# Performance work log

Measured on AMD Instinct MI355X. Metric: run time of the kernel, lower is better.

Reference implementation:

```python
import jax, jax.numpy as jnp
import numpy as np

B, T, C, L = 256, 512, 512, 64  # batch, timesteps, num_classes (blank = C-1), max label len
NEG = -1e30   # log-space 'minus infinity' that is safe under fp arithmetic
EPS = 1e-7    # keras.backend.epsilon() used by ctc_batch_cost


def _ctc_loss(log_probs, labels, in_len, lab_len, blank):
    """CTC negative log-likelihood via the forward (alpha) DP in log space.
    log_probs: [T, B, C] log probabilities; labels: [B, L] int; in_len, lab_len: [B] int.
    Returns [B] loss. Matches tf.nn.ctc_loss with merge_repeated=True, blank=C-1."""
    Tn, Bn, Cn = log_probs.shape
    Ln = labels.shape[1]
    S = 2 * Ln + 1  # extended label: blank, l1, blank, l2, ..., blank
    ext = jnp.full((Bn, S), blank, dtype=labels.dtype).at[:, 1::2].set(labels)  # [B,S]
    # skip transition s-2 -> s allowed iff ext[s] != blank and ext[s] != ext[s-2]
    allow = jnp.concatenate(
        [jnp.zeros((Bn, 2), dtype=bool),
         (ext[:, 2:] != blank) & (ext[:, 2:] != ext[:, :-2])], axis=1)  # [B,S]
    # emission log-probs for each extended-label position at every step: [T,B,S]
    emit = log_probs[:, jnp.arange(Bn)[:, None], ext]

    alpha0 = (jnp.full((Bn, S), NEG, dtype=log_probs.dtype)
              .at[:, 0].set(emit[0, :, 0])
              .at[:, 1].set(emit[0, :, 1]))

    def step(alpha, e):
        a1 = jnp.pad(alpha, ((0, 0), (1, 0)), constant_values=NEG)[:, :-1]
        a2 = jnp.pad(alpha, ((0, 0), (2, 0)), constant_values=NEG)[:, :-2]
        a2 = jnp.where(allow, a2, NEG)
        new = jax.nn.logsumexp(jnp.stack([alpha, a1, a2], axis=0), axis=0) + e
        return new, new

    _, alphas = jax.lax.scan(step, alpha0, emit[1:])
    alphas = jnp.concatenate([alpha0[None], alphas], axis=0)  # [T,B,S]
    # alpha at the last valid timestep of each sample
    final = alphas[in_len - 1, jnp.arange(Bn)]  # [B,S]
    i1 = (2 * lab_len)[:, None]       # last blank position
    i2 = (2 * lab_len - 1)[:, None]   # last label position
    last = jnp.concatenate(
        [jnp.take_along_axis(final, i1, axis=1),
         jnp.take_along_axis(final, i2, axis=1)], axis=1)  # [B,2]
    return -jax.nn.logsumexp(last, axis=1)  # [B]


def setup_inputs() -> dict:
    key = jax.random.key(0)
    k1, k2 = jax.random.split(key)
    # model output is a softmax distribution over classes (keras ctc_batch_cost contract)
    y_pred = jax.nn.softmax(jax.random.normal(k1, (B, T, C), dtype=jnp.float32), axis=-1)
    y_true = jax.random.randint(k2, (B, L), 0, C - 1, dtype=jnp.int32)  # never blank (C-1)
    input_length = jnp.full((B, 1), T, dtype=jnp.int32)
    label_length = jnp.full((B, 1), L, dtype=jnp.int32)
    return {"y_true": y_true, "y_pred": y_pred,
            "input_length": input_length, "label_length": label_length}


def reference(y_true, y_pred, input_length, label_length):
    # keras.backend.ctc_batch_cost: log(transpose(y_pred) + eps), blank = num_classes-1
    log_probs = jnp.log(jnp.transpose(y_pred, (1, 0, 2)) + EPS)  # [T,B,C]
    loss = _ctc_loss(log_probs, y_true, input_length[:, 0], label_length[:, 0], C - 1)
    return loss[:, None]  # [B,1], matching ctc_batch_cost
```

## Files before the change

### kernel.cpp

```cpp
#include <hip/hip_runtime.h>


constexpr int Bc = 256, Tc = 512, Cc = 512, Lc = 64;
constexpr int BLANK = Cc - 1;
constexpr float EPSF = 1e-7f;
constexpr float NEGI = -1e30f;
constexpr float LN2 = 0.6931471805599453f;
constexpr int SR = 64;
constexpr int NSEG = Tc / SR;
constexpr int NW = 8;
constexpr int NPROD = NW - 1;

__device__ __forceinline__ float exp2_hw(float x) { return __builtin_amdgcn_exp2f(x); }
__device__ __forceinline__ float log2_hw(float x) { return __builtin_amdgcn_logf(x); }

__device__ __forceinline__ float lse2(float a, float b) {
    float m = fmaxf(a, b);
    return m + log2_hw(exp2_hw(a - m) + exp2_hw(b - m));
}
__device__ __forceinline__ float lse3(float a, float b, float c) {
    float m = fmaxf(fmaxf(a, b), c);
    return m + log2_hw(exp2_hw(a - m) + exp2_hw(b - m) + exp2_hw(c - m));
}

__global__ __launch_bounds__(NW * 64, 1) void ctc_fwd(
    const int* __restrict__ labels,
    const float* __restrict__ yp,
    const int* __restrict__ in_len,
    const int* __restrict__ lab_len,
    float* __restrict__ out)
{
    __shared__ float sL[2][SR * 64];
    __shared__ float sB[2][SR];

    const int b = blockIdx.x;
    const int tid = threadIdx.x;
    const int lane = tid & 63;
    const int wave = tid >> 6;

    const float* __restrict__ row0 = yp + (size_t)b * (size_t)(Tc * Cc);

    const int lab = labels[b * Lc + lane];
    const int labPrev = __shfl_up(lab, 1);
    const bool allow = (lane >= 1 && lab != BLANK && lab != labPrev);

    int til = in_len[b];  if (til > Tc) til = Tc;
    const int lln = lab_len[b];

    auto fillRow = [&](int buf, int t, int r) {
        float v  = row0[(size_t)t * Cc + lab];
        float vb = row0[(size_t)t * Cc + BLANK];
        sL[buf][r * 64 + lane] = log2_hw(v + EPSF);
        if (lane == 0) sB[buf][r] = log2_hw(vb + EPSF);
    };

    #pragma unroll 2
    for (int r = wave; r < SR; r += NW) fillRow(0, r, r);

    float aB, aL, aH = NEGI;
    {
        float eb0 = log2_hw(row0[BLANK] + EPSF);
        float el0 = log2_hw(row0[lab] + EPSF);
        aB = (lane == 0) ? eb0 : NEGI;
        aL = (lane == 0) ? el0 : NEGI;
    }

    __syncthreads();

    for (int s = 0; s < NSEG; ++s) {
        const int buf = s & 1;
        if (wave == 0) {
            #pragma unroll 8
            for (int k = 0; k < SR; ++k) {
                int t = s * SR + k;
                float el = sL[buf][k * 64 + lane];
                float eb = sB[buf][k];

                float lp = __shfl_up(aL, 1);
                lp = (lane == 0) ? NEGI : lp;
                float lpm = allow ? lp : NEGI;

                float nB = lse2(aB, lp) + eb;
                float nL = lse3(aL, aB, lpm) + el;
                float nH = lse2(aH, aL) + eb;
                if (t >= 1 && t < til) { aB = nB; aL = nL; aH = nH; }
            }
        } else if (s + 1 < NSEG) {
            const int tb = (s + 1) * SR;
            #pragma unroll 2
            for (int r = wave - 1; r < SR; r += NPROD) fillRow(buf ^ 1, tb + r, r);
        }
        __syncthreads();
    }

    if (wave == 0) {
        float v1a = __shfl(aB, lln & 63);
        float v1b = __shfl(aH, 63);
        float v1 = (lln >= 64) ? v1b : v1a;
        float v2 = (lln >= 1) ? __shfl(aL, (lln - 1) & 63) : NEGI;
        if (lane == 0) out[b] = -LN2 * lse2(v1, v2);
    }
}

extern "C" void kernel_launch(void* const* d_in, const int* in_sizes, int n_in,
                              void* d_out, int out_size, void* d_ws, size_t ws_size,
                              hipStream_t stream) {
    const int*   y_true       = (const int*)d_in[0];
    const float* y_pred       = (const float*)d_in[1];
    const int*   input_length = (const int*)d_in[2];
    const int*   label_length = (const int*)d_in[3];
    float*       out          = (float*)d_out;

    ctc_fwd<<<Bc, NW * 64, 0, stream>>>(y_true, y_pred, input_length, label_length, out);
}
```

Before: 387.8 us.

## Stage full probability rows via coalesced float4 loads into shared memory

Replaces the scattered per-label gathers from global memory with all 512 threads streaming whole time-step rows (16 steps × 512 classes) into a double-buffered shared tile using coalesced float4 loads held in registers. The DP wave then gathers label and blank probabilities from shared memory and computes the log itself. Segment length drops from 64 to 16. The change reads the full row (8x more bytes than needed) and adds more syncs, in exchange for coalesced access and no uncoalesced gather latency. It also moves the log computation onto the serial DP path.

```diff
diff --git a/kernel.cpp b/kernel.cpp
--- a/kernel.cpp
+++ b/kernel.cpp
@@ -6,10 +6,11 @@
 constexpr float EPSF = 1e-7f;
 constexpr float NEGI = -1e30f;
 constexpr float LN2 = 0.6931471805599453f;
-constexpr int SR = 64;
+constexpr int SR = 16;
 constexpr int NSEG = Tc / SR;
-constexpr int NW = 8;
-constexpr int NPROD = NW - 1;
+constexpr int NT = 512;
+constexpr int F4_SEG = SR * Cc / 4;
+constexpr int F4_THR = F4_SEG / NT;
 
 __device__ __forceinline__ float exp2_hw(float x) { return __builtin_amdgcn_exp2f(x); }
 __device__ __forceinline__ float log2_hw(float x) { return __builtin_amdgcn_logf(x); }
@@ -23,15 +24,14 @@
     return m + log2_hw(exp2_hw(a - m) + exp2_hw(b - m) + exp2_hw(c - m));
 }
 
-__global__ __launch_bounds__(NW * 64, 1) void ctc_fwd(
+__global__ __launch_bounds__(NT, 1) void ctc_fwd(
     const int* __restrict__ labels,
     const float* __restrict__ yp,
     const int* __restrict__ in_len,
     const int* __restrict__ lab_len,
     float* __restrict__ out)
 {
-    __shared__ float sL[2][SR * 64];
-    __shared__ float sB[2][SR];
+    __shared__ float F[2][SR * Cc];
 
     const int b = blockIdx.x;
     const int tid = threadIdx.x;
@@ -47,18 +47,15 @@
     int til = in_len[b];  if (til > Tc) til = Tc;
     const int lln = lab_len[b];
 
-    auto fillRow = [&](int buf, int t, int r) {
-        float v  = row0[(size_t)t * Cc + lab];
-        float vb = row0[(size_t)t * Cc + BLANK];
-        sL[buf][r * 64 + lane] = log2_hw(v + EPSF);
-        if (lane == 0) sB[buf][r] = log2_hw(vb + EPSF);
-    };
-
-    #pragma unroll 2
-    for (int r = wave; r < SR; r += NW) fillRow(0, r, r);
+    {
+        const float4* __restrict__ src = (const float4*)row0;
+        float4* dst = (float4*)F[0];
+        #pragma unroll
+        for (int i = 0; i < F4_THR; ++i) dst[tid + NT * i] = src[tid + NT * i];
+    }
 
     float aB, aL, aH = NEGI;
-    {
+    if (wave == 0) {
         float eb0 = log2_hw(row0[BLANK] + EPSF);
         float el0 = log2_hw(row0[lab] + EPSF);
         aB = (lane == 0) ? eb0 : NEGI;
@@ -69,12 +66,22 @@
 
     for (int s = 0; s < NSEG; ++s) {
         const int buf = s & 1;
+        const bool more = (s + 1 < NSEG);
+
+        float4 v[F4_THR];
+        if (more) {
+            const float4* __restrict__ src =
+                (const float4*)(row0 + (size_t)(s + 1) * SR * Cc);
+            #pragma unroll
+            for (int i = 0; i < F4_THR; ++i) v[i] = src[tid + NT * i];
+        }
+
         if (wave == 0) {
-            #pragma unroll 8
+            #pragma unroll 4
             for (int k = 0; k < SR; ++k) {
                 int t = s * SR + k;
-                float el = sL[buf][k * 64 + lane];
-                float eb = sB[buf][k];
+                float el = log2_hw(F[buf][k * Cc + lab] + EPSF);
+                float eb = log2_hw(F[buf][k * Cc + BLANK] + EPSF);
 
                 float lp = __shfl_up(aL, 1);
                 lp = (lane == 0) ? NEGI : lp;
@@ -85,10 +92,12 @@
                 float nH = lse2(aH, aL) + eb;
                 if (t >= 1 && t < til) { aB = nB; aL = nL; aH = nH; }
             }
-        } else if (s + 1 < NSEG) {
-            const int tb = (s + 1) * SR;
-            #pragma unroll 2
-            for (int r = wave - 1; r < SR; r += NPROD) fillRow(buf ^ 1, tb + r, r);
+        }
+
+        if (more) {
+            float4* dst = (float4*)F[buf ^ 1];
+            #pragma unroll
+            for (int i = 0; i < F4_THR; ++i) dst[tid + NT * i] = v[i];
         }
         __syncthreads();
     }
@@ -111,5 +120,5 @@
     const int*   label_length = (const int*)d_in[3];
     float*       out          = (float*)d_out;
 
-    ctc_fwd<<<Bc, NW * 64, 0, stream>>>(y_true, y_pred, input_length, label_length, out);
+    ctc_fwd<<<Bc, NT, 0, stream>>>(y_true, y_pred, input_length, label_length, out);
 }
```

After: 390.4 us. About the same (+0.7%).
